# Kernel optimization log

Hardware: AMD Instinct MI355X
Metric: run time of the kernel (lower is better)

## Reference

```python
import jax, jax.numpy as jnp
import numpy as np


def _gather_tree(step_ids, parent_ids, max_seq_lens, end_token):
    """Vectorized beam-search backtrace.

    step_ids, parent_ids: [max_len, batch, beam] int32
    max_seq_lens: [batch] int32
    Returns beams: [max_len, batch, beam]
    """
    max_len, batch, beam = step_ids.shape
    # current back-pointer per (batch, beam); starts at own beam index
    own = jnp.broadcast_to(jnp.arange(beam, dtype=step_ids.dtype), (batch, beam))
    msl = jnp.minimum(max_seq_lens, max_len)[:, None]  # [batch, 1]

    def step(cur, xs):
        t, s_t, p_t = xs  # s_t, p_t: [batch, beam]
        active = t < msl  # [batch, 1] -> broadcasts over beam
        tok = jnp.where(active, jnp.take_along_axis(s_t, cur, axis=1), end_token)
        new_cur = jnp.where(active, jnp.take_along_axis(p_t, cur, axis=1), cur)
        return new_cur, tok

    ts = jnp.arange(max_len - 1, -1, -1, dtype=msl.dtype)
    _, toks = jax.lax.scan(step, own, (ts, step_ids[::-1], parent_ids[::-1]))
    beams = toks[::-1]  # [max_len, batch, beam]
    # once an end_token is produced, every later position becomes end_token
    ended = jnp.cumsum((beams == end_token).astype(jnp.int32), axis=0) > 0
    return jnp.where(ended, jnp.asarray(end_token, beams.dtype), beams)


def setup_inputs() -> dict:
    key = jax.random.key(0)
    k1, k2, k3 = jax.random.split(key, 3)
    max_len, batch, beam = 256, 4096, 8
    output_ids = jax.random.randint(k1, (max_len, batch, beam), 0, 32000, dtype=jnp.int32)
    parent_ids = jax.random.randint(k2, (max_len, batch, beam), 0, beam, dtype=jnp.int32)
    out_seq_lens = jax.random.randint(k3, (batch, beam), 0, max_len, dtype=jnp.int32)
    return {
        "output_ids": output_ids,
        "parent_ids": parent_ids,
        "out_seq_lens": out_seq_lens,
        "end_id": 2,
    }


def reference(output_ids, parent_ids, out_seq_lens, end_id):
    # finalize(): per-batch max decode length over beams
    max_lens = jnp.max(out_seq_lens, axis=1)  # [batch]
    ids = _gather_tree(output_ids, parent_ids, max_lens, end_id)  # [max_len, batch, beam]
    ids = jnp.transpose(ids, (1, 2, 0))  # einsum 'ijk->jki' -> [batch, beam, max_len]
    lengths = jnp.sum((ids != end_id).astype(output_ids.dtype), axis=-1)  # [batch, beam]
    return ids, lengths
```

## Files before the change

### kernel.cpp

```cpp
#include <hip/hip_runtime.h>


constexpr int MAX_LEN = 256;
constexpr int BATCH   = 4096;
constexpr int BEAM    = 8;
constexpr int NCHAIN  = BATCH * BEAM;
constexpr int PITCH   = 65;

__global__ __launch_bounds__(64)
void gather_tree_kernel(const int* __restrict__ step_ids,
                        const int* __restrict__ parent_ids,
                        const int* __restrict__ seq_lens,
                        const int* __restrict__ end_id_p,
                        int* __restrict__ out_ids,
                        int* __restrict__ out_lens)
{
    __shared__ int toks[MAX_LEN * PITCH];

    const int lane = threadIdx.x;
    const int bj0  = blockIdx.x * 64;
    const int bj   = bj0 + lane;
    const int j    = bj & (BEAM - 1);
    const int grp  = lane & ~(BEAM - 1);
    const int end_tok = *end_id_p;

    int sl = seq_lens[bj];
    sl = max(sl, __shfl_xor(sl, 1));
    sl = max(sl, __shfl_xor(sl, 2));
    sl = max(sl, __shfl_xor(sl, 4));
    const int msl = min(sl, MAX_LEN);

    int cur = j;
    int first_end = MAX_LEN;
    int idx = (MAX_LEN - 1) * NCHAIN + bj;

    #pragma unroll 16
    for (int t = MAX_LEN - 1; t >= 0; --t, idx -= NCHAIN) {
        int s = step_ids[idx];
        int p = parent_ids[idx];
        int src = grp + cur;
        int tokg = __shfl(s, src);
        int pg   = __shfl(p, src);
        bool active = t < msl;
        int tok = active ? tokg : end_tok;
        cur = active ? (pg & (BEAM - 1)) : cur;
        if (tok == end_tok) first_end = t;
        toks[t * PITCH + lane] = tok;
    }

    __syncthreads();

    for (int c = 0; c < 64; ++c) {
        int fe = __shfl(first_end, c);
        int obase = (bj0 + c) * MAX_LEN;
        #pragma unroll
        for (int k = 0; k < 4; ++k) {
            int t = k * 64 + lane;
            int v = toks[t * PITCH + c];
            out_ids[obase + t] = (t < fe) ? v : end_tok;
        }
    }

    out_lens[bj] = first_end;
}

extern "C" void kernel_launch(void* const* d_in, const int* in_sizes, int n_in,
                              void* d_out, int out_size, void* d_ws, size_t ws_size,
                              hipStream_t stream)
{
    const int* step_ids   = (const int*)d_in[0];
    const int* parent_ids = (const int*)d_in[1];
    const int* seq_lens   = (const int*)d_in[2];
    const int* end_id     = (const int*)d_in[3];

    int* out_ids  = (int*)d_out;
    int* out_lens = (int*)d_out + MAX_LEN * NCHAIN;

    gather_tree_kernel<<<NCHAIN / 64, 64, 0, stream>>>(
        step_ids, parent_ids, seq_lens, end_id, out_ids, out_lens);
}
```

Baseline: 117.8 us.

## Split backtrace across four waves via composed parent maps per time segment

Each 64-chain block now uses four wavefronts, each handling a 64-step time segment. Within a segment, each wave packs the 8-beam parent permutation into a 24-bit map and records the per-step beam indices, so the segment can be walked without knowing the starting beam. Segment end maps are then composed across waves to find each wave's entry beam, and the recorded history resolves the tokens from shared memory. This parallelises the serial 256-step dependency chain and raises per-block parallelism, at the cost of extra shuffles, a small history buffer in shared memory and two block barriers.

```diff
diff --git a/kernel.cpp b/kernel.cpp
--- a/kernel.cpp
+++ b/kernel.cpp
@@ -6,8 +6,9 @@
 constexpr int BEAM    = 8;
 constexpr int NCHAIN  = BATCH * BEAM;
 constexpr int PITCH   = 65;
+constexpr unsigned ID_MAP = 0xFAC688u;
 
-__global__ __launch_bounds__(64)
+__global__ __launch_bounds__(256)
 void gather_tree_kernel(const int* __restrict__ step_ids,
                         const int* __restrict__ parent_ids,
                         const int* __restrict__ seq_lens,
@@ -15,53 +16,85 @@
                         int* __restrict__ out_ids,
                         int* __restrict__ out_lens)
 {
-    __shared__ int toks[MAX_LEN * PITCH];
+    __shared__ int      s_tile[MAX_LEN * PITCH];
+    __shared__ unsigned hist[4 * 8 * 64];
+    __shared__ unsigned segmap[4 * 8];
+    __shared__ int      fe_buf[4 * 64];
 
-    const int lane = threadIdx.x;
-    const int bj0  = blockIdx.x * 64;
-    const int bj   = bj0 + lane;
-    const int j    = bj & (BEAM - 1);
-    const int grp  = lane & ~(BEAM - 1);
+    const int tid   = threadIdx.x;
+    const int w     = tid >> 6;
+    const int lane  = tid & 63;
+    const int b_loc = lane >> 3;
+    const int h     = lane & 7;
+    const int bj0   = blockIdx.x * 64;
+    const int tbase = w * 64;
     const int end_tok = *end_id_p;
 
-    int sl = seq_lens[bj];
+    int sl = seq_lens[bj0 + lane];
     sl = max(sl, __shfl_xor(sl, 1));
     sl = max(sl, __shfl_xor(sl, 2));
     sl = max(sl, __shfl_xor(sl, 4));
     const int msl = min(sl, MAX_LEN);
 
-    int cur = j;
-    int first_end = MAX_LEN;
-    int idx = (MAX_LEN - 1) * NCHAIN + bj;
-
-    #pragma unroll 16
-    for (int t = MAX_LEN - 1; t >= 0; --t, idx -= NCHAIN) {
-        int s = step_ids[idx];
-        int p = parent_ids[idx];
-        int src = grp + cur;
-        int tokg = __shfl(s, src);
-        int pg   = __shfl(p, src);
-        bool active = t < msl;
-        int tok = active ? tokg : end_tok;
-        cur = active ? (pg & (BEAM - 1)) : cur;
-        if (tok == end_tok) first_end = t;
-        toks[t * PITCH + lane] = tok;
+    int cur = h;
+    for (int kb = 56; kb >= 0; kb -= 8) {
+        unsigned hw = 0;
+        #pragma unroll
+        for (int i = 7; i >= 0; --i) {
+            const int t = tbase + kb + i;
+            const int gidx = t * NCHAIN + bj0 + lane;
+            int s = step_ids[gidx];
+            int p = parent_ids[gidx];
+            s_tile[t * PITCH + lane] = s;
+            unsigned m = (unsigned)(p & 7) << (3 * h);
+            m |= (unsigned)__shfl_xor((int)m, 1);
+            m |= (unsigned)__shfl_xor((int)m, 2);
+            m |= (unsigned)__shfl_xor((int)m, 4);
+            const unsigned me = (t < msl) ? m : ID_MAP;
+            hw |= (unsigned)cur << (3 * i);
+            cur = (me >> (3 * cur)) & 7;
+        }
+        hist[(w * 8 + (kb >> 3)) * 64 + lane] = hw;
     }
+    unsigned fm = (unsigned)cur << (3 * h);
+    fm |= (unsigned)__shfl_xor((int)fm, 1);
+    fm |= (unsigned)__shfl_xor((int)fm, 2);
+    fm |= (unsigned)__shfl_xor((int)fm, 4);
+    if (h == 0) segmap[w * 8 + b_loc] = fm;
 
     __syncthreads();
 
-    for (int c = 0; c < 64; ++c) {
-        int fe = __shfl(first_end, c);
-        int obase = (bj0 + c) * MAX_LEN;
+    int e = h;
+    for (int ww = 3; ww > w; --ww)
+        e = (segmap[ww * 8 + b_loc] >> (3 * e)) & 7;
+
+    int fe = MAX_LEN;
+    for (int kb = 0; kb < 64; kb += 8) {
+        const unsigned hw = hist[(w * 8 + (kb >> 3)) * 64 + b_loc * 8 + e];
         #pragma unroll
-        for (int k = 0; k < 4; ++k) {
-            int t = k * 64 + lane;
-            int v = toks[t * PITCH + c];
-            out_ids[obase + t] = (t < fe) ? v : end_tok;
+        for (int i = 0; i < 8; ++i) {
+            const int t = tbase + kb + i;
+            const int c = (hw >> (3 * i)) & 7;
+            int tok = s_tile[t * PITCH + b_loc * 8 + c];
+            tok = (t < msl) ? tok : end_tok;
+            if (tok == end_tok) fe = min(fe, t);
+            s_tile[t * PITCH + lane] = tok;
         }
     }
+    fe_buf[w * 64 + lane] = fe;
 
-    out_lens[bj] = first_end;
+    __syncthreads();
+
+    const int feg = min(min(fe_buf[lane], fe_buf[64 + lane]),
+                        min(fe_buf[128 + lane], fe_buf[192 + lane]));
+    if (w == 0) out_lens[bj0 + lane] = feg;
+
+    const int t = tbase + lane;
+    for (int c0 = 0; c0 < 64; ++c0) {
+        const int fec = __shfl(feg, c0);
+        const int v = s_tile[t * PITCH + c0];
+        out_ids[(bj0 + c0) * MAX_LEN + t] = (t < fec) ? v : end_tok;
+    }
 }
 
 extern "C" void kernel_launch(void* const* d_in, const int* in_sizes, int n_in,
@@ -76,6 +109,6 @@
     int* out_ids  = (int*)d_out;
     int* out_lens = (int*)d_out + MAX_LEN * NCHAIN;
 
-    gather_tree_kernel<<<NCHAIN / 64, 64, 0, stream>>>(
+    gather_tree_kernel<<<NCHAIN / 64, 256, 0, stream>>>(
         step_ids, parent_ids, seq_lens, end_id, out_ids, out_lens);
 }
```

Result: faster. 109.6 us (-7.0%).
